# Kernel optimization log

Measured on AMD Instinct MI355X. Metric: run time of the kernel, lower is better.

## Reference

```python
import jax, jax.numpy as jnp
import numpy as np

TEMP = 0.025
BN_EPS = 1e-5


def _attention(a, W_in, b_in, g, beta, rm, rv, W_out, b_out):
    # a: (b, n1, n2, P, Q); 1x1 conv over the Q 'channel' dim, gate, softmax over P.
    m = a.mean(axis=3)                                   # (b,n1,n2,Q)
    t = jnp.einsum('bnmq,kq->bnmk', m, W_in) + b_in      # (b,n1,n2,K)
    t = jax.nn.relu((t - rm) / jnp.sqrt(rv + BN_EPS) * g + beta)
    t = jnp.einsum('bnmk,qk->bnmq', t, W_out) + b_out    # (b,n1,n2,Q)
    s = jnp.mean(a * t[:, :, :, None, :], axis=-1)       # (b,n1,n2,P)
    return jax.nn.softmax(s / TEMP, axis=-1) + 1.0


def _cam_forward(zf, xf, conv1_w, conv1_b, bn1_g, bn1_b, bn1_rm, bn1_rv,
                 conv2_w, conv2_b, conv3_w, conv3_b, bn3_g, bn3_b, bn3_rm, bn3_rv,
                 conv4_w, conv4_b):
    out1, out2 = [], []
    L = zf.shape[0]
    for l in range(L):  # small fixed loop over feature levels
        f1, f2 = zf[l], xf[l]
        b, c, h1, w1 = f1.shape
        h2, w2 = f2.shape[2], f2.shape[3]
        P, Q = h1 * w1, h2 * w2
        f1s = jnp.stack([f1.reshape(b, c, P)] * 2, axis=1)   # (b,2,c,P)
        f2s = jnp.stack([f2.reshape(b, c, Q)] * 2, axis=1)   # (b,2,c,Q)
        f1n = f1s / jnp.maximum(jnp.linalg.norm(f1s, axis=2, keepdims=True), 1e-12)
        f2n = f2s / jnp.maximum(jnp.linalg.norm(f2s, axis=2, keepdims=True), 1e-12)
        a1 = jnp.einsum('bncp,bmcq->bnmpq', f1n, f2n)        # (b,2,2,P,Q)
        att1 = _attention(a1, conv1_w, conv1_b, bn1_g, bn1_b, bn1_rm, bn1_rv,
                          conv2_w, conv2_b)                  # (b,2,2,P)
        att2 = _attention(a1.swapaxes(3, 4), conv3_w, conv3_b, bn3_g, bn3_b,
                          bn3_rm, bn3_rv, conv4_w, conv4_b)  # (b,2,2,Q)
        # mean over the (n1,n2)=(2,2) pair grid without materializing (b,2,2,c,HW)
        o1 = jnp.einsum('bncp,bnmp->bcp', f1s, att1) / 4.0
        o2 = jnp.einsum('bmcq,bnmq->bcq', f2s, att2) / 4.0
        out1.append(o1.reshape(b, c, h1, w1))
        out2.append(o2.reshape(b, c, h2, w2))
    return (jnp.stack(out1), jnp.stack(out2))


def setup_inputs() -> dict:
    key = jax.random.key(0)
    ks = jax.random.split(key, 12)
    L, B, C = 3, 32, 256
    inp = {
        'zf': jax.random.normal(ks[0], (L, B, C, 7, 7), jnp.float32),
        'xf': jax.random.normal(ks[1], (L, B, C, 31, 31), jnp.float32),
        'conv1_w': jax.random.normal(ks[2], (31, 961), jnp.float32) * np.sqrt(2.0 / 31),
        'conv1_b': jax.random.normal(ks[3], (31,), jnp.float32) * 0.05,
        'bn1_g': jax.random.uniform(ks[4], (31,), jnp.float32, 0.5, 1.5),
        'bn1_b': jax.random.normal(ks[5], (31,), jnp.float32) * 0.05,
        'bn1_rm': jnp.zeros((31,), jnp.float32),
        'bn1_rv': jnp.ones((31,), jnp.float32),
        'conv2_w': jax.random.normal(ks[6], (961, 31), jnp.float32) * np.sqrt(2.0 / 961),
        'conv2_b': jax.random.normal(ks[7], (961,), jnp.float32) * 0.05,
        'conv3_w': jax.random.normal(ks[8], (7, 49), jnp.float32) * np.sqrt(2.0 / 7),
        'conv3_b': jax.random.normal(ks[9], (7,), jnp.float32) * 0.05,
        'bn3_g': jax.random.uniform(ks[10], (7,), jnp.float32, 0.5, 1.5),
        'bn3_b': jax.random.normal(ks[11], (7,), jnp.float32) * 0.05,
        'bn3_rm': jnp.zeros((7,), jnp.float32),
        'bn3_rv': jnp.ones((7,), jnp.float32),
        'conv4_w': jax.random.normal(jax.random.fold_in(key, 100), (49, 7), jnp.float32) * np.sqrt(2.0 / 49),
        'conv4_b': jax.random.normal(jax.random.fold_in(key, 101), (49,), jnp.float32) * 0.05,
    }
    return inp


def reference(zf, xf, conv1_w, conv1_b, bn1_g, bn1_b, bn1_rm, bn1_rv,
              conv2_w, conv2_b, conv3_w, conv3_b, bn3_g, bn3_b, bn3_rm, bn3_rv,
              conv4_w, conv4_b):
    return _cam_forward(zf, xf, conv1_w, conv1_b, bn1_g, bn1_b, bn1_rm, bn1_rv,
                        conv2_w, conv2_b, conv3_w, conv3_b, bn3_g, bn3_b,
                        bn3_rm, bn3_rv, conv4_w, conv4_b)
```

## Files before the change

kernel.cpp:

```cpp
#include <hip/hip_runtime.h>
#include <math.h>

#define NLB 96
#define CC  256
#define PP  49
#define QQ  961
#define TEMP_INV 40.0f
#define BN_EPS 1e-5f

#define N1 (NLB*CC*PP)
#define N2 (NLB*CC*QQ)

typedef __attribute__((ext_vector_type(8))) short bf16x8;
typedef __attribute__((ext_vector_type(4))) float f32x4;
typedef __attribute__((ext_vector_type(8))) unsigned short ushort8;

__device__ inline unsigned short f2bf(float x) {
    unsigned int u = __float_as_uint(x);
    unsigned int r = (u + 0x7fffu + ((u >> 16) & 1u)) >> 16;
    return (unsigned short)r;
}

__global__ __launch_bounds__(256) void prep_z(
    const float* __restrict__ zf, unsigned short* __restrict__ f1T,
    float* __restrict__ inv1_ws, float* __restrict__ mrow_ws)
{
    const int lb = blockIdx.x;
    if (threadIdx.x < PP) mrow_ws[lb * PP + threadIdx.x] = 0.f;

    const float* __restrict__ f1 = zf + (size_t)lb * CC * PP;
    const int p  = threadIdx.x >> 2;
    const int qu = threadIdx.x & 3;
    const int c0 = qu * 64;
    float ss = 0.f;
    ushort8* dst = (ushort8*)(f1T + ((size_t)lb * 64 + p) * CC + c0);
#pragma unroll
    for (int s = 0; s < 8; ++s) {
        unsigned short tmp[8];
#pragma unroll
        for (int j = 0; j < 8; ++j) {
            const float v = (p < PP) ? f1[(size_t)(c0 + s * 8 + j) * PP + p] : 0.f;
            ss = fmaf(v, v, ss);
            tmp[j] = f2bf(v);
        }
        dst[s] = *(ushort8*)tmp;
    }
    ss += __shfl_xor(ss, 1, 64);
    ss += __shfl_xor(ss, 2, 64);
    if (qu == 0) inv1_ws[lb * 64 + p] = (p < PP) ? 1.0f / fmaxf(sqrtf(ss), 1e-12f) : 0.f;
}

#define LOAD_KC(KC, RR)                                                        \
    {                                                                          \
        const float* __restrict__ s0 =                                         \
            f2 + (size_t)((KC) * 64 + g4 * 8) * QQ + qcl;                      \
        _Pragma("unroll")                                                      \
        for (int t = 0; t < 16; ++t) {                                         \
            const int ks = t >> 3, j = t & 7;                                  \
            RR[t] = qv ? s0[(size_t)(ks * 32 + j) * QQ] : 0.f;                 \
        }                                                                      \
    }

#define COMP_KC(KC, RR)                                                        \
    {                                                                          \
        bf16x8 af[4][2];                                                       \
        _Pragma("unroll")                                                      \
        for (int mt = 0; mt < 4; ++mt)                                         \
            _Pragma("unroll")                                                  \
            for (int ks = 0; ks < 2; ++ks)                                     \
                af[mt][ks] = *(const bf16x8*)&f1L[(mt * 16 + l15) * 264 +      \
                                                  (KC) * 64 + ks * 32 + g4 * 8];\
        _Pragma("unroll")                                                      \
        for (int ks = 0; ks < 2; ++ks) {                                       \
            unsigned short us[8];                                              \
            _Pragma("unroll")                                                  \
            for (int j = 0; j < 8; ++j) {                                      \
                const float v = RR[ks * 8 + j];                                \
                ss2 = fmaf(v, v, ss2);                                         \
                us[j] = f2bf(v);                                               \
            }                                                                  \
            const bf16x8 bfr = *(const bf16x8*)us;                             \
            _Pragma("unroll")                                                  \
            for (int mt = 0; mt < 4; ++mt)                                     \
                acc[mt] = __builtin_amdgcn_mfma_f32_16x16x32_bf16(             \
                    af[mt][ks], bfr, acc[mt], 0, 0, 0);                        \
        }                                                                      \
    }

__global__ __launch_bounds__(512) void corr_mfma(
    const unsigned short* __restrict__ f1T, const float* __restrict__ xf,
    const float* __restrict__ inv1_ws,
    float* __restrict__ A_all, float* __restrict__ mcol_ws,
    float* __restrict__ mrow_ws)
{
    const int ng = blockIdx.x;
    const int lb = blockIdx.y;
    const int tid  = threadIdx.x;
    const int lane = tid & 63;
    const int wave = tid >> 6;
    const int g4   = lane >> 4;
    const int l15  = lane & 15;

    const float* __restrict__ f2 = xf + (size_t)lb * CC * QQ;

    __shared__ __align__(16) unsigned short f1L[64 * 264];
    __shared__ float inv1L[64];

    for (int i = tid; i < 64 * 32; i += 512) {
        const int row = i >> 5, seg = i & 31;
        *(ushort8*)&f1L[row * 264 + seg * 8] =
            *(const ushort8*)&f1T[((size_t)lb * 64 + row) * CC + seg * 8];
    }
    if (tid < 64) inv1L[tid] = inv1_ws[lb * 64 + tid];
    __syncthreads();

    const int qg = ng * 128 + wave * 16 + l15;
    const bool qv = (qg < QQ);
    const int qcl = qv ? qg : 0;

    f32x4 acc[4];
#pragma unroll
    for (int mt = 0; mt < 4; ++mt) acc[mt] = (f32x4)0.f;
    float ss2 = 0.f;

    float rrA[16], rrB[16];
    LOAD_KC(0, rrA)
    LOAD_KC(1, rrB)
    COMP_KC(0, rrA)
    LOAD_KC(2, rrA)
    COMP_KC(1, rrB)
    LOAD_KC(3, rrB)
    COMP_KC(2, rrA)
    COMP_KC(3, rrB)

    float ssf = ss2;
    ssf += __shfl_xor(ssf, 16, 64);
    ssf += __shfl_xor(ssf, 32, 64);
    const float iv2 = 1.0f / fmaxf(sqrtf(ssf), 1e-12f);

    float* __restrict__ Aout = A_all + (size_t)lb * PP * QQ;
    float vv[16];
    float cs = 0.f;
#pragma unroll
    for (int mt = 0; mt < 4; ++mt)
#pragma unroll
        for (int r = 0; r < 4; ++r) {
            const int p = mt * 16 + g4 * 4 + r;
            const float v = acc[mt][r] * inv1L[p] * iv2;
            vv[mt * 4 + r] = v;
            cs += v;
            if (p < PP && qv) Aout[(size_t)p * QQ + qg] = v;
        }
    cs += __shfl_xor(cs, 16, 64);
    cs += __shfl_xor(cs, 32, 64);
    if ((lane < 16) && qv) mcol_ws[lb * QQ + qg] = cs;
#pragma unroll
    for (int mt = 0; mt < 4; ++mt)
#pragma unroll
        for (int r = 0; r < 4; ++r) {
            const int p = mt * 16 + g4 * 4 + r;
            float s = vv[mt * 4 + r];
            s += __shfl_xor(s, 1, 64);
            s += __shfl_xor(s, 2, 64);
            s += __shfl_xor(s, 4, 64);
            s += __shfl_xor(s, 8, 64);
            if (((lane & 15) == 0) && p < PP) atomicAdd(&mrow_ws[lb * PP + p], s);
        }
}

__global__ __launch_bounds__(512) void attn_kernel(
    const float* __restrict__ A_all,
    const float* __restrict__ mcol_ws, const float* __restrict__ mrow_ws,
    const float* __restrict__ W1, const float* __restrict__ b1,
    const float* __restrict__ g1, const float* __restrict__ bb1,
    const float* __restrict__ rm1, const float* __restrict__ rv1,
    const float* __restrict__ W2, const float* __restrict__ b2,
    const float* __restrict__ W3, const float* __restrict__ b3,
    const float* __restrict__ g3, const float* __restrict__ bb3,
    const float* __restrict__ rm3, const float* __restrict__ rv3,
    const float* __restrict__ W4, const float* __restrict__ b4,
    float* __restrict__ att1_ws, float* __restrict__ att2_ws)
{
    const int lb = blockIdx.x;
    const float* __restrict__ A = A_all + (size_t)lb * PP * QQ;
    const int tid  = threadIdx.x;
    const int lane = tid & 63;
    const int wv   = tid >> 6;

    __shared__ float mcolL[QQ];
    __shared__ float mrowL[PP];
    __shared__ float taL[31], tbL[7];
    __shared__ float t2aL[QQ], t2bL[PP];
    __shared__ float s2sL[QQ];
    __shared__ float s1L[PP];
    __shared__ float redM[8], redS[8];

    for (int q = tid; q < QQ; q += 512) mcolL[q] = mcol_ws[lb * QQ + q] * (1.0f / PP);
    if (tid < PP) mrowL[tid] = mrow_ws[lb * PP + tid] * (1.0f / QQ);
    __syncthreads();

    if (tid < 31 * 16) {
        const int k = tid >> 4, sub = tid & 15;
        float s = 0.f;
        for (int q = sub; q < QQ; q += 16) s = fmaf(mcolL[q], W1[k * QQ + q], s);
        s += __shfl_xor(s, 1, 64); s += __shfl_xor(s, 2, 64);
        s += __shfl_xor(s, 4, 64); s += __shfl_xor(s, 8, 64);
        if (sub == 0) {
            float t = s + b1[k];
            t = (t - rm1[k]) * rsqrtf(rv1[k] + BN_EPS) * g1[k] + bb1[k];
            taL[k] = fmaxf(t, 0.f);
        }
    }
    if (tid < 7 * 8) {
        const int k = tid >> 3, sub = tid & 7;
        float s = 0.f;
        for (int p = sub; p < PP; p += 8) s = fmaf(mrowL[p], W3[k * PP + p], s);
        s += __shfl_xor(s, 1, 64); s += __shfl_xor(s, 2, 64); s += __shfl_xor(s, 4, 64);
        if (sub == 0) {
            float t = s + b3[k];
            t = (t - rm3[k]) * rsqrtf(rv3[k] + BN_EPS) * g3[k] + bb3[k];
            tbL[k] = fmaxf(t, 0.f);
        }
    }
    __syncthreads();

    for (int q = tid; q < QQ; q += 512) {
        float s = b2[q];
#pragma unroll
        for (int k = 0; k < 31; ++k) s = fmaf(taL[k], W2[q * 31 + k], s);
        t2aL[q] = s;
    }
    if (tid < PP) {
        float s = b4[tid];
#pragma unroll
        for (int k = 0; k < 7; ++k) s = fmaf(tbL[k], W4[tid * 7 + k], s);
        t2bL[tid] = s;
    }
    __syncthreads();

    for (int q = tid; q < QQ; q += 512) {
        float s = 0.f;
#pragma unroll
        for (int p = 0; p < PP; ++p) s = fmaf(A[(size_t)p * QQ + q], t2bL[p], s);
        s2sL[q] = s * (1.0f / PP) * TEMP_INV;
    }
    for (int p = wv; p < PP; p += 8) {
        float s = 0.f;
        for (int q = lane; q < QQ; q += 64) s = fmaf(A[(size_t)p * QQ + q], t2aL[q], s);
        for (int off = 32; off > 0; off >>= 1) s += __shfl_xor(s, off, 64);
        if (lane == 0) s1L[p] = s * (1.0f / QQ) * TEMP_INV;
    }
    __syncthreads();

    if (wv == 0) {
        const float v = (lane < PP) ? s1L[lane] : -3.4e38f;
        float m = v;
        for (int off = 32; off > 0; off >>= 1) m = fmaxf(m, __shfl_xor(m, off, 64));
        const float e = (lane < PP) ? expf(v - m) : 0.f;
        float sum = e;
        for (int off = 32; off > 0; off >>= 1) sum += __shfl_xor(sum, off, 64);
        if (lane < PP) att1_ws[lb * PP + lane] = e / sum + 1.0f;
    }

    float lm = -3.4e38f;
    for (int q = tid; q < QQ; q += 512) lm = fmaxf(lm, s2sL[q]);
    for (int off = 32; off > 0; off >>= 1) lm = fmaxf(lm, __shfl_xor(lm, off, 64));
    if (lane == 0) redM[wv] = lm;
    __syncthreads();
    float gm = redM[0];
#pragma unroll
    for (int i = 1; i < 8; ++i) gm = fmaxf(gm, redM[i]);
    float ls = 0.f;
    for (int q = tid; q < QQ; q += 512) ls += expf(s2sL[q] - gm);
    for (int off = 32; off > 0; off >>= 1) ls += __shfl_xor(ls, off, 64);
    if (lane == 0) redS[wv] = ls;
    __syncthreads();
    float tot = 0.f;
#pragma unroll
    for (int i = 0; i < 8; ++i) tot += redS[i];
    const float rinv = 1.0f / tot;
    for (int q = tid; q < QQ; q += 512)
        att2_ws[lb * QQ + q] = expf(s2sL[q] - gm) * rinv + 1.0f;
}

template <int INNER>
__global__ __launch_bounds__(256) void scale_kernel(
    const float* __restrict__ in, const float* __restrict__ att,
    float* __restrict__ out, int n4)
{
    const int i = blockIdx.x * 256 + threadIdx.x;
    if (i >= n4) return;
    const float4 v = reinterpret_cast<const float4*>(in)[i];
    const float* vv = reinterpret_cast<const float*>(&v);
    float4 o;
    float* ov = reinterpret_cast<float*>(&o);
    const int g = i * 4;
#pragma unroll
    for (int j = 0; j < 4; ++j) {
        const int gg = g + j;
        const int lb = gg / (CC * INNER);
        const int x  = gg % INNER;
        ov[j] = vv[j] * att[lb * INNER + x];
    }
    reinterpret_cast<float4*>(out)[i] = o;
}

extern "C" void kernel_launch(void* const* d_in, const int* in_sizes, int n_in,
                              void* d_out, int out_size, void* d_ws, size_t ws_size,
                              hipStream_t stream)
{
    const float* zf  = (const float*)d_in[0];
    const float* xf  = (const float*)d_in[1];
    const float* W1  = (const float*)d_in[2];
    const float* b1  = (const float*)d_in[3];
    const float* g1  = (const float*)d_in[4];
    const float* bb1 = (const float*)d_in[5];
    const float* rm1 = (const float*)d_in[6];
    const float* rv1 = (const float*)d_in[7];
    const float* W2  = (const float*)d_in[8];
    const float* b2  = (const float*)d_in[9];
    const float* W3  = (const float*)d_in[10];
    const float* b3  = (const float*)d_in[11];
    const float* g3  = (const float*)d_in[12];
    const float* bb3 = (const float*)d_in[13];
    const float* rm3 = (const float*)d_in[14];
    const float* rv3 = (const float*)d_in[15];
    const float* W4  = (const float*)d_in[16];
    const float* b4  = (const float*)d_in[17];

    char* wsb = (char*)d_ws;
    unsigned short* f1T = (unsigned short*)wsb;
    float* fbase = (float*)(f1T + (size_t)NLB * 64 * CC);
    float* A     = fbase;
    float* att1  = A + (size_t)NLB * PP * QQ;
    float* att2  = att1 + (size_t)NLB * PP;
    float* mcol  = att2 + (size_t)NLB * QQ;
    float* mrow  = mcol + (size_t)NLB * QQ;
    float* inv1  = mrow + (size_t)NLB * PP;

    float* out1 = (float*)d_out;
    float* out2 = out1 + N1;

    prep_z<<<NLB, 256, 0, stream>>>(zf, f1T, inv1, mrow);

    dim3 gcorr(8, NLB);
    corr_mfma<<<gcorr, 512, 0, stream>>>(f1T, xf, inv1, A, mcol, mrow);

    attn_kernel<<<NLB, 512, 0, stream>>>(A, mcol, mrow,
        W1, b1, g1, bb1, rm1, rv1, W2, b2,
        W3, b3, g3, bb3, rm3, rv3, W4, b4,
        att1, att2);

    const int n4_1 = N1 / 4;
    const int n4_2 = N2 / 4;
    scale_kernel<PP><<<(n4_1 + 255) / 256, 256, 0, stream>>>(zf, att1, out1, n4_1);
    scale_kernel<QQ><<<(n4_2 + 255) / 256, 256, 0, stream>>>(xf, att2, out2, n4_2);
}
```

Before: 140.2 us.

## Stage xf tiles into LDS with global_load_lds double buffering

The correlation kernel used to gather f2 values straight into registers with per-lane strided loads. It now copies each 64-channel by 128-q chunk into LDS with direct global-to-LDS dword loads, so each 64-lane row load is contiguous. Two LDS buffers are alternated, with a block barrier between stages so the next chunk loads while the current one is computed. This adds 64 KB of LDS per block and extra barriers, which may limit occupancy. Out-of-range q columns are clamped on load and zeroed at output.

```diff
diff --git a/kernel.cpp b/kernel.cpp
--- a/kernel.cpp
+++ b/kernel.cpp
@@ -21,6 +21,13 @@
     return (unsigned short)r;
 }
 
+__device__ __forceinline__ void gload_lds4(const float* g, float* l) {
+    __builtin_amdgcn_global_load_lds(
+        (const __attribute__((address_space(1))) void*)g,
+        (__attribute__((address_space(3))) void*)l,
+        4, 0, 0);
+}
+
 __global__ __launch_bounds__(256) void prep_z(
     const float* __restrict__ zf, unsigned short* __restrict__ f1T,
     float* __restrict__ inv1_ws, float* __restrict__ mrow_ws)
@@ -50,18 +57,22 @@
     if (qu == 0) inv1_ws[lb * 64 + p] = (p < PP) ? 1.0f / fmaxf(sqrtf(ss), 1e-12f) : 0.f;
 }
 
-#define LOAD_KC(KC, RR)                                                        \
+#define STAGE(BUF, KC)                                                         \
     {                                                                          \
-        const float* __restrict__ s0 =                                         \
-            f2 + (size_t)((KC) * 64 + g4 * 8) * QQ + qcl;                      \
+        const int c0s = (KC) * 64 + wave * 8;                                  \
         _Pragma("unroll")                                                      \
-        for (int t = 0; t < 16; ++t) {                                         \
-            const int ks = t >> 3, j = t & 7;                                  \
-            RR[t] = qv ? s0[(size_t)(ks * 32 + j) * QQ] : 0.f;                 \
+        for (int r8 = 0; r8 < 8; ++r8) {                                       \
+            _Pragma("unroll")                                                  \
+            for (int h = 0; h < 2; ++h) {                                      \
+                const int qi = ng * 128 + h * 64 + lane;                       \
+                const int qc2 = qi < QQ ? qi : QQ - 1;                         \
+                gload_lds4(f2 + (size_t)(c0s + r8) * QQ + qc2,                 \
+                           &BUF[(wave * 8 + r8) * 128 + h * 64]);              \
+            }                                                                  \
         }                                                                      \
     }
 
-#define COMP_KC(KC, RR)                                                        \
+#define COMPS(BUF, KC)                                                         \
     {                                                                          \
         bf16x8 af[4][2];                                                       \
         _Pragma("unroll")                                                      \
@@ -75,7 +86,7 @@
             unsigned short us[8];                                              \
             _Pragma("unroll")                                                  \
             for (int j = 0; j < 8; ++j) {                                      \
-                const float v = RR[ks * 8 + j];                                \
+                const float v = BUF[(ks * 32 + g4 * 8 + j) * 128 + wq + l15];  \
                 ss2 = fmaf(v, v, ss2);                                         \
                 us[j] = f2bf(v);                                               \
             }                                                                  \
@@ -100,12 +111,16 @@
     const int wave = tid >> 6;
     const int g4   = lane >> 4;
     const int l15  = lane & 15;
+    const int wq   = wave * 16;
 
     const float* __restrict__ f2 = xf + (size_t)lb * CC * QQ;
 
     __shared__ __align__(16) unsigned short f1L[64 * 264];
     __shared__ float inv1L[64];
-
+    __shared__ __align__(16) float bufA[64 * 128];
+    __shared__ __align__(16) float bufB[64 * 128];
+
+    STAGE(bufA, 0)
     for (int i = tid; i < 64 * 32; i += 512) {
         const int row = i >> 5, seg = i & 31;
         *(ushort8*)&f1L[row * 264 + seg * 8] =
@@ -114,24 +129,24 @@
     if (tid < 64) inv1L[tid] = inv1_ws[lb * 64 + tid];
     __syncthreads();
 
-    const int qg = ng * 128 + wave * 16 + l15;
+    const int qg = ng * 128 + wq + l15;
     const bool qv = (qg < QQ);
-    const int qcl = qv ? qg : 0;
 
     f32x4 acc[4];
 #pragma unroll
     for (int mt = 0; mt < 4; ++mt) acc[mt] = (f32x4)0.f;
     float ss2 = 0.f;
 
-    float rrA[16], rrB[16];
-    LOAD_KC(0, rrA)
-    LOAD_KC(1, rrB)
-    COMP_KC(0, rrA)
-    LOAD_KC(2, rrA)
-    COMP_KC(1, rrB)
-    LOAD_KC(3, rrB)
-    COMP_KC(2, rrA)
-    COMP_KC(3, rrB)
+    STAGE(bufB, 1)
+    COMPS(bufA, 0)
+    __syncthreads();
+    STAGE(bufA, 2)
+    COMPS(bufB, 1)
+    __syncthreads();
+    STAGE(bufB, 3)
+    COMPS(bufA, 2)
+    __syncthreads();
+    COMPS(bufB, 3)
 
     float ssf = ss2;
     ssf += __shfl_xor(ssf, 16, 64);
@@ -146,7 +161,7 @@
 #pragma unroll
         for (int r = 0; r < 4; ++r) {
             const int p = mt * 16 + g4 * 4 + r;
-            const float v = acc[mt][r] * inv1L[p] * iv2;
+            const float v = qv ? acc[mt][r] * inv1L[p] * iv2 : 0.f;
             vv[mt * 4 + r] = v;
             cs += v;
             if (p < PP && qv) Aout[(size_t)p * QQ + qg] = v;
```

New measurement: 146.7 us. 4.7% more time.
